# Kernel tuning notes

Measured on AMD Instinct MI355X. Metric: run time of the kernel, lower is better.

## Reference

```python
import jax, jax.numpy as jnp
import numpy as np

SEED_THRESHOLD = 0.5
DUPLICATE_THRESHOLD = 0.8


def setup_inputs() -> dict:
    key = jax.random.key(0)
    k1, k2 = jax.random.split(key)
    B, Q, C = 16, 1800, 256
    return {
        "query_signatures": jax.random.normal(k1, (B, Q, C), dtype=jnp.float32),
        "query_seed_logits": jax.random.normal(k2, (B, Q), dtype=jnp.float32),
    }


def _cc_labels(adj):
    """Connected-component labels via min-label propagation. adj: [Q,Q] bool (symmetric).
    Label of each node = smallest node index in its component. Unconnected nodes keep own index."""
    Q = adj.shape[0]
    labels0 = jnp.arange(Q, dtype=jnp.int32)

    def cond(state):
        return state[1]

    def body(state):
        labels, _ = state
        nbr_min = jnp.min(jnp.where(adj, labels[None, :], Q), axis=1)
        new = jnp.minimum(labels, nbr_min)
        return new, jnp.any(new != labels)

    labels, _ = jax.lax.while_loop(cond, body, (labels0, jnp.bool_(True)))
    return labels


def reference(query_signatures, query_seed_logits):
    sig = query_signatures                     # [B,Q,C]
    B, Q, C = sig.shape
    qidx = jnp.arange(Q)

    scores = jax.nn.sigmoid(query_seed_logits.astype(jnp.float32))   # [B,Q]
    selected = scores >= SEED_THRESHOLD                               # [B,Q]
    # fallback: if no query selected in an image, select the argmax-score query
    empty = ~jnp.any(selected, axis=1)                                # [B]
    fb = jnp.argmax(scores, axis=1)                                   # [B]
    selected = selected | (empty[:, None] & (qidx[None, :] == fb[:, None]))

    # cosine pairwise similarity
    nrm = jnp.linalg.norm(sig, axis=-1, keepdims=True)
    nsig = sig / jnp.maximum(nrm, 1e-12)
    sim = jnp.einsum("bqc,bkc->bqk", nsig, nsig)                      # [B,Q,Q]

    adj = (sim >= DUPLICATE_THRESHOLD) & selected[:, :, None] & selected[:, None, :]
    adj = adj.at[:, qidx, qidx].set(selected)                         # diag = selected

    labels = jax.vmap(_cc_labels)(adj)                                # [B,Q] int32

    # a label slot l hosts a component iff node l is selected and is its own component min
    active = selected & (labels == qidx[None, :].astype(labels.dtype))  # [B,Q]

    # per-component best-score member (components visited in ascending min-index order,
    # matching the torch BFS-from-ascending-node order)
    member = (labels[:, None, :] == qidx[None, :, None].astype(labels.dtype)) & selected[:, None, :]  # [B,Ql,Qn]
    masked_scores = jnp.where(member, scores[:, None, :], -jnp.inf)
    best = jnp.argmax(masked_scores, axis=2)                          # [B,Q] node index of best per label
    best_sig = jnp.take_along_axis(sig, best[..., None], axis=1)      # [B,Q,C]
    best_score = jnp.take_along_axis(scores, best, axis=1)            # [B,Q]

    # compact active components to the front (pad to Q, the static max)
    pos = jnp.cumsum(active, axis=1) - 1
    dest = jnp.where(active, pos, Q)                                  # inactive -> dropped

    seed_signatures = jax.vmap(
        lambda d, v: jnp.zeros((Q, C), sig.dtype).at[d].set(v, mode="drop")
    )(dest, best_sig)
    seed_scores = jax.vmap(
        lambda d, v: jnp.zeros((Q,), scores.dtype).at[d].set(v, mode="drop")
    )(dest, best_score)

    num_seeds = jnp.sum(active, axis=1)
    pad_mask = qidx[None, :] < num_seeds[:, None]
    return seed_signatures, pad_mask, seed_scores
```

## Files before the change

### kernel.cpp

```cpp
#include <hip/hip_runtime.h>
#include <hip/hip_bf16.h>
#include <stdint.h>

#define B_ 16
#define Q_ 1800
#define C_ 256
#define WPR 29
#define QPAD 1856
#define TBK 15
#define NTRI 120
#define OUT_SIG_ELEMS (B_*Q_*C_)

typedef unsigned long long u64;
typedef unsigned int u32;
typedef __attribute__((ext_vector_type(8))) short bf16x8;
typedef __attribute__((ext_vector_type(4))) float f32x4;

__global__ __launch_bounds__(256)
void k_compact(const float* __restrict__ logits,
               int* __restrict__ sel_idx, int* __restrict__ sel_cnt,
               int* __restrict__ dirty) {
  int b = blockIdx.x, t = threadIdx.x;
  int lane = t & 63, wid = t >> 6;
  __shared__ int wsum[4];
  __shared__ int s_tot;
  __shared__ u64 kw[4];
  const float* lgb = logits + b * Q_;
  if (t == 0) dirty[b] = 0;

  int f[8]; int cnt = 0;
  #pragma unroll
  for (int e = 0; e < 8; ++e) {
    int q = t * 8 + e; int fl = 0;
    if (q < Q_) fl = (lgb[q] >= 0.0f) ? 1 : 0;
    f[e] = fl; cnt += fl;
  }
  int incl = cnt;
  #pragma unroll
  for (int d = 1; d < 64; d <<= 1) {
    int v = __shfl_up(incl, d, 64);
    if (lane >= d) incl += v;
  }
  if (lane == 63) wsum[wid] = incl;
  __syncthreads();
  if (t == 0) {
    int acc = 0;
    #pragma unroll
    for (int i = 0; i < 4; ++i) { int v = wsum[i]; wsum[i] = acc; acc += v; }
    s_tot = acc;
  }
  __syncthreads();
  int excl = wsum[wid] + incl - cnt;
  int total = s_tot;

  if (total > 0) {
    #pragma unroll
    for (int e = 0; e < 8; ++e) {
      if (f[e]) { sel_idx[b * Q_ + excl] = t * 8 + e; excl++; }
    }
    if (t == 0) sel_cnt[b] = total;
  } else {
    u64 mk = 0;
    for (int q = t; q < Q_; q += 256) {
      float sc = 1.0f / (1.0f + expf(-lgb[q]));
      u64 key = ((u64)__float_as_uint(sc) << 32) | (u32)(~(u32)q);
      mk = (mk > key) ? mk : key;
    }
    #pragma unroll
    for (int d = 1; d < 64; d <<= 1) { u64 o = __shfl_xor(mk, d, 64); mk = (o > mk) ? o : mk; }
    if (lane == 0) kw[wid] = mk;
    __syncthreads();
    if (t == 0) {
      u64 m2 = kw[0];
      #pragma unroll
      for (int i = 1; i < 4; ++i) m2 = (kw[i] > m2) ? kw[i] : m2;
      sel_idx[b * Q_] = (int)(~(u32)m2);
      sel_cnt[b] = 1;
    }
  }
}

__global__ __launch_bounds__(256)
void k_prepg(const float* __restrict__ sig, const float* __restrict__ logits,
             const int* __restrict__ sel_idx, const int* __restrict__ sel_cnt,
             unsigned short* __restrict__ nsig, u32* __restrict__ rowmin,
             float* __restrict__ out_sig, float* __restrict__ out_mask,
             float* __restrict__ out_scores) {
  int b = blockIdx.y;
  int p = blockIdx.x * 4 + (threadIdx.x >> 6);
  int lane = threadIdx.x & 63;
  int S = sel_cnt[b];
  int Spad = (S + 63) & ~63;

  if (p < Spad && lane == 0) rowmin[b * QPAD + p] = 0xFFFFFFFFu;

  if (p < S) {
    int row = sel_idx[b * Q_ + p];
    const float* src = sig + ((size_t)b * Q_ + row) * C_;
    float4 v = *reinterpret_cast<const float4*>(src + lane * 4);

    float* orow = out_sig + ((size_t)b * Q_ + p) * C_;
    *reinterpret_cast<float4*>(orow + lane * 4) = v;
    if (lane == 0) {
      out_mask[b * Q_ + p] = 1.0f;
      out_scores[b * Q_ + p] = 1.0f / (1.0f + expf(-logits[b * Q_ + row]));
    }

    float ss = v.x * v.x + v.y * v.y + v.z * v.z + v.w * v.w;
    #pragma unroll
    for (int m = 32; m; m >>= 1) ss += __shfl_xor(ss, m, 64);
    float inv = 1.0f / fmaxf(sqrtf(ss), 1e-12f);
    __hip_bfloat16 h0 = __float2bfloat16(v.x * inv);
    __hip_bfloat16 h1 = __float2bfloat16(v.y * inv);
    __hip_bfloat16 h2 = __float2bfloat16(v.z * inv);
    __hip_bfloat16 h3 = __float2bfloat16(v.w * inv);
    unsigned short u0, u1, u2, u3;
    __builtin_memcpy(&u0, &h0, 2); __builtin_memcpy(&u1, &h1, 2);
    __builtin_memcpy(&u2, &h2, 2); __builtin_memcpy(&u3, &h3, 2);
    uint2 wv;
    wv.x = (u32)u0 | ((u32)u1 << 16);
    wv.y = (u32)u2 | ((u32)u3 << 16);
    *reinterpret_cast<uint2*>(nsig + ((size_t)b * QPAD + p) * C_ + lane * 4) = wv;
  } else {
    if (p < Spad)
      *reinterpret_cast<uint2*>(nsig + ((size_t)b * QPAD + p) * C_ + lane * 4) =
          make_uint2(0u, 0u);
    if (p < Q_) {
      float* orow = out_sig + ((size_t)b * Q_ + p) * C_;
      *reinterpret_cast<float4*>(orow + lane * 4) = make_float4(0.f, 0.f, 0.f, 0.f);
      if (lane == 0) {
        out_mask[b * Q_ + p] = 0.0f;
        out_scores[b * Q_ + p] = 0.0f;
      }
    }
  }
}

__global__ __launch_bounds__(256)
void k_prep(const float* __restrict__ sig, const int* __restrict__ sel_idx,
            const int* __restrict__ sel_cnt, unsigned short* __restrict__ nsig,
            u32* __restrict__ rowmin) {
  int b = blockIdx.y;
  int p = blockIdx.x * 4 + (threadIdx.x >> 6);
  int lane = threadIdx.x & 63;
  int S = sel_cnt[b];
  int Spad = (S + 63) & ~63;
  if (p >= Spad) return;
  if (lane == 0) rowmin[b * QPAD + p] = 0xFFFFFFFFu;
  unsigned short* dst = nsig + ((size_t)b * QPAD + p) * C_;
  if (p >= S) {
    *reinterpret_cast<uint2*>(dst + lane * 4) = make_uint2(0u, 0u);
    return;
  }
  int row = sel_idx[b * Q_ + p];
  const float* src = sig + ((size_t)b * Q_ + row) * C_;
  float4 v = *reinterpret_cast<const float4*>(src + lane * 4);
  float ss = v.x * v.x + v.y * v.y + v.z * v.z + v.w * v.w;
  #pragma unroll
  for (int m = 32; m; m >>= 1) ss += __shfl_xor(ss, m, 64);
  float inv = 1.0f / fmaxf(sqrtf(ss), 1e-12f);
  __hip_bfloat16 h0 = __float2bfloat16(v.x * inv);
  __hip_bfloat16 h1 = __float2bfloat16(v.y * inv);
  __hip_bfloat16 h2 = __float2bfloat16(v.z * inv);
  __hip_bfloat16 h3 = __float2bfloat16(v.w * inv);
  unsigned short u0, u1, u2, u3;
  __builtin_memcpy(&u0, &h0, 2); __builtin_memcpy(&u1, &h1, 2);
  __builtin_memcpy(&u2, &h2, 2); __builtin_memcpy(&u3, &h3, 2);
  uint2 wv;
  wv.x = (u32)u0 | ((u32)u1 << 16);
  wv.y = (u32)u2 | ((u32)u3 << 16);
  *reinterpret_cast<uint2*>(dst + lane * 4) = wv;
}

__global__ __launch_bounds__(256)
void k_sim(const unsigned short* __restrict__ nsig, const int* __restrict__ sel_cnt,
           u64* __restrict__ adj, u32* __restrict__ rowmin,
           int* __restrict__ dirty) {
  int lin = blockIdx.x;
  int b = lin & 15;
  int u = lin >> 4, tib = 0;
  while (u >= TBK - tib) { u -= TBK - tib; ++tib; }
  int tjb = tib + u;
  int S = sel_cnt[b];
  if (tjb * 128 >= S) return;
  const bool diag = (tib == tjb);

  __shared__ uint4 Alds[2048];
  __shared__ uint4 Blds[2048];
  __shared__ u64 adjtile[4][64];

  const int t = threadIdx.x;
  const int wv = t >> 6, lane = t & 63;
  const int lr = lane & 15, lg = lane >> 4;

  const int i1 = tib * 128 + (wv >> 1) * 64;
  const int j1 = tjb * 128 + (wv & 1) * 64;
  const bool live = (i1 < S) && (j1 < S);

  const char* gbase = (const char*)(nsig + (size_t)b * QPAD * C_);
  const char* arow = gbase + (size_t)tib * 128 * 512;
  const char* brow = gbase + (size_t)tjb * 128 * 512;

  f32x4 acc[4][4];
  #pragma unroll
  for (int rs = 0; rs < 4; ++rs)
    #pragma unroll
    for (int cg = 0; cg < 4; ++cg) acc[rs][cg] = (f32x4){0.f, 0.f, 0.f, 0.f};

  const int ra0 = (wv >> 1) * 64;
  const int rb0 = (wv & 1) * 64;
  const char* Bbase = reinterpret_cast<const char*>(diag ? Alds : Blds);

  for (int kh = 0; kh < 2; ++kh) {
    #pragma unroll
    for (int it = 0; it < 8; ++it) {
      int o = it * 4096 + t * 16;
      int r = o >> 8;
      int w = o & 255;
      int sw = o ^ ((r & 7) << 4);
      uint4 va = *reinterpret_cast<const uint4*>(arow + (size_t)r * 512 + kh * 256 + w);
      Alds[sw >> 4] = va;
      if (!diag) {
        uint4 vb = *reinterpret_cast<const uint4*>(brow + (size_t)r * 512 + kh * 256 + w);
        Blds[sw >> 4] = vb;
      }
    }
    __syncthreads();
    if (live) {
      #pragma unroll
      for (int ks = 0; ks < 4; ++ks) {
        bf16x8 af[4], bf[4];
        #pragma unroll
        for (int rs = 0; rs < 4; ++rs) {
          int r = ra0 + rs * 16 + lr;
          int byte = r * 256 + ((ks * 64 + lg * 16) ^ ((r & 7) << 4));
          af[rs] = *reinterpret_cast<const bf16x8*>(
              reinterpret_cast<const char*>(Alds) + byte);
        }
        #pragma unroll
        for (int cg = 0; cg < 4; ++cg) {
          int r = rb0 + cg * 16 + lr;
          int byte = r * 256 + ((ks * 64 + lg * 16) ^ ((r & 7) << 4));
          bf[cg] = *reinterpret_cast<const bf16x8*>(Bbase + byte);
        }
        #pragma unroll
        for (int rs = 0; rs < 4; ++rs)
          #pragma unroll
          for (int cg = 0; cg < 4; ++cg)
            acc[rs][cg] = __builtin_amdgcn_mfma_f32_16x16x32_bf16(
                af[rs], bf[cg], acc[rs][cg], 0, 0, 0);
      }
    }
    __syncthreads();
  }

  if (!live) return;
  adjtile[wv][lane] = 0ull;
  #pragma unroll
  for (int rs = 0; rs < 4; ++rs) {
    #pragma unroll
    for (int j = 0; j < 4; ++j) {
      u64 bits = 0ull;
      if (acc[rs][0][j] >= 0.8f) bits |= 1ull << (0  + lr);
      if (acc[rs][1][j] >= 0.8f) bits |= 1ull << (16 + lr);
      if (acc[rs][2][j] >= 0.8f) bits |= 1ull << (32 + lr);
      if (acc[rs][3][j] >= 0.8f) bits |= 1ull << (48 + lr);
      if (bits) atomicOr(&adjtile[wv][rs * 16 + lg * 4 + j], bits);
    }
  }
  int gi = i1 + lane;
  u64 word = adjtile[wv][lane];
  u64 selfbit = (i1 == j1) ? (1ull << lane) : 0ull;
  bool offd = (gi < S) && ((word & ~selfbit) != 0ull);
  if (__any(offd) && lane == 0) atomicOr(&dirty[b], 1);
  if (gi < S) {
    adj[((size_t)b * Q_ + gi) * WPR + (j1 >> 6)] = word;
    if (word) atomicMin(&rowmin[b * QPAD + gi], (u32)(j1 + __builtin_ctzll(word)));
  }
  if (!diag) {
    u64 tw = 0ull;
    for (int i = 0; i < 64; ++i)
      tw |= ((adjtile[wv][i] >> lane) & 1ull) << i;
    int gj = j1 + lane;
    if (gj < S) {
      adj[((size_t)b * Q_ + gj) * WPR + (i1 >> 6)] = tw;
      if (tw) atomicMin(&rowmin[b * QPAD + gj], (u32)(i1 + __builtin_ctzll(tw)));
    }
  }
}

__global__ __launch_bounds__(1024)
void k_fix(const float* __restrict__ sig, const float* __restrict__ logits,
           const int* __restrict__ sel_idx, const int* __restrict__ sel_cnt,
           const u64* __restrict__ adj, const u32* __restrict__ rowmin,
           const int* __restrict__ dirty,
           int* __restrict__ best_idx, float* __restrict__ best_sc,
           float* __restrict__ out_sig, float* __restrict__ out_mask,
           float* __restrict__ out_scores) {
  int b = blockIdx.x;
  if (!dirty[b]) return;
  int t = threadIdx.x;
  int lane = t & 63, wid = t >> 6;
  __shared__ int lab[Q_];
  __shared__ int lab2[Q_];
  __shared__ u64 best[Q_];
  __shared__ int wsum[16];
  __shared__ int s_tot;
  __shared__ int s_changed;

  int S = sel_cnt[b];
  int nw = (S + 63) >> 6;
  const u64* arow0 = adj + (size_t)b * Q_ * WPR;

  for (int s = t; s < S; s += 1024) {
    u32 m = rowmin[b * QPAD + s];
    lab[s] = (int)(((u32)s < m) ? (u32)s : m);
  }
  __syncthreads();
  for (int iter = 0; iter < Q_ + 2; ++iter) {
    if (t == 0) s_changed = 0;
    __syncthreads();
    for (int s = t; s < S; s += 1024) {
      int m = lab[s];
      const u64* row = arow0 + (size_t)s * WPR;
      for (int w = 0; w < nw; ++w) {
        u64 msk = row[w];
        while (msk) {
          int j = (w << 6) + __builtin_ctzll(msk);
          int lj = lab[j];
          m = (lj < m) ? lj : m;
          msk &= msk - 1;
        }
      }
      lab2[s] = m;
      if (m != lab[s]) s_changed = 1;
    }
    __syncthreads();
    int ch = s_changed;
    for (int s = t; s < S; s += 1024) lab[s] = lab2[s];
    __syncthreads();
    if (!ch) break;
  }

  for (int s = t; s < S; s += 1024) best[s] = 0ull;
  __syncthreads();
  const int* sidx = sel_idx + b * Q_;
  for (int s = t; s < S; s += 1024) {
    int orig = sidx[s];
    float sc = 1.0f / (1.0f + expf(-logits[b * Q_ + orig]));
    u64 key = ((u64)__float_as_uint(sc) << 32) | (u32)(~(u32)orig);
    atomicMax(&best[lab[s]], key);
  }
  __syncthreads();

  int f[2]; int cnt = 0;
  #pragma unroll
  for (int e = 0; e < 2; ++e) {
    int s = t * 2 + e;
    int fl = (s < S && lab[s] == s) ? 1 : 0;
    f[e] = fl; cnt += fl;
  }
  int incl = cnt;
  #pragma unroll
  for (int d = 1; d < 64; d <<= 1) {
    int v = __shfl_up(incl, d, 64);
    if (lane >= d) incl += v;
  }
  if (lane == 63) wsum[wid] = incl;
  __syncthreads();
  if (t == 0) {
    int acc = 0;
    #pragma unroll
    for (int i = 0; i < 16; ++i) { int v = wsum[i]; wsum[i] = acc; acc += v; }
    s_tot = acc;
  }
  __syncthreads();
  int excl = wsum[wid] + incl - cnt;
  #pragma unroll
  for (int e = 0; e < 2; ++e) {
    if (f[e]) {
      int s = t * 2 + e;
      u64 key = best[s];
      best_idx[b * Q_ + excl] = (int)(~(u32)key);
      best_sc[b * Q_ + excl] = __uint_as_float((u32)(key >> 32));
      excl++;
    }
  }
  __syncthreads();
  int n = s_tot;

  for (int p = wid; p < Q_; p += 16) {
    float* orow = out_sig + ((size_t)b * Q_ + p) * C_;
    if (p < n) {
      int row = best_idx[b * Q_ + p];
      float4 v = *reinterpret_cast<const float4*>(sig + ((size_t)b * Q_ + row) * C_ + lane * 4);
      *reinterpret_cast<float4*>(orow + lane * 4) = v;
      if (lane == 0) {
        out_mask[b * Q_ + p] = 1.0f;
        out_scores[b * Q_ + p] = best_sc[b * Q_ + p];
      }
    } else {
      *reinterpret_cast<float4*>(orow + lane * 4) = make_float4(0.f, 0.f, 0.f, 0.f);
      if (lane == 0) {
        out_mask[b * Q_ + p] = 0.0f;
        out_scores[b * Q_ + p] = 0.0f;
      }
    }
  }
}

__global__ __launch_bounds__(256)
void k_ccgather(const float* __restrict__ sig, const float* __restrict__ logits,
                const int* __restrict__ sel_idx, const int* __restrict__ sel_cnt,
                const u64* __restrict__ adj, const u32* __restrict__ rowmin,
                float* __restrict__ out_sig, float* __restrict__ out_mask,
                float* __restrict__ out_scores) {
  const int b = blockIdx.y, g = blockIdx.x;
  const int t = threadIdx.x, lane = t & 63, wid = t >> 6;
  __shared__ int lab[Q_];
  __shared__ int lab2[Q_];
  __shared__ u64 best[Q_];
  __shared__ int wsum[4];
  __shared__ int s_tot;
  __shared__ int s_dirty;

  const int S = sel_cnt[b];
  if (t == 0) s_dirty = 0;
  __syncthreads();
  for (int s = t; s < S; s += 256)
    if (rowmin[b * QPAD + s] != (u32)s) s_dirty = 1;
  __syncthreads();

  const int p = g * 4 + wid;
  float* orow = out_sig + ((size_t)b * Q_ + p) * C_;

  if (!s_dirty) {
    if (p < S) {
      int row = sel_idx[b * Q_ + p];
      float4 v = *reinterpret_cast<const float4*>(sig + ((size_t)b * Q_ + row) * C_ + lane * 4);
      *reinterpret_cast<float4*>(orow + lane * 4) = v;
      if (lane == 0) {
        out_mask[b * Q_ + p] = 1.0f;
        out_scores[b * Q_ + p] = 1.0f / (1.0f + expf(-logits[b * Q_ + row]));
      }
    } else {
      *reinterpret_cast<float4*>(orow + lane * 4) = make_float4(0.f, 0.f, 0.f, 0.f);
      if (lane == 0) {
        out_mask[b * Q_ + p] = 0.0f;
        out_scores[b * Q_ + p] = 0.0f;
      }
    }
    return;
  }

  const int nw = (S + 63) >> 6;
  const u64* arow0 = adj + (size_t)b * Q_ * WPR;
  __shared__ int s_chg;

  if (t == 0) s_chg = 1;
  for (int s = t; s < S; s += 256) {
    u32 m = rowmin[b * QPAD + s];
    lab[s] = (int)(((u32)s < m) ? (u32)s : m);
  }
  __syncthreads();
  for (int iter = 0; iter < Q_ + 2; ++iter) {
    if (t == 0) s_chg = 0;
    __syncthreads();
    for (int s = t; s < S; s += 256) {
      int m = lab[s];
      const u64* row = arow0 + (size_t)s * WPR;
      for (int w = 0; w < nw; ++w) {
        u64 msk = row[w];
        while (msk) {
          int j = (w << 6) + __builtin_ctzll(msk);
          int lj = lab[j];
          m = (lj < m) ? lj : m;
          msk &= msk - 1;
        }
      }
      lab2[s] = m;
      if (m != lab[s]) s_chg = 1;
    }
    __syncthreads();
    int ch = s_chg;
    for (int s = t; s < S; s += 256) lab[s] = lab2[s];
    __syncthreads();
    if (!ch) break;
  }

  for (int s = t; s < S; s += 256) best[s] = 0ull;
  __syncthreads();
  const int* sidx = sel_idx + b * Q_;
  for (int s = t; s < S; s += 256) {
    int orig = sidx[s];
    float sc = 1.0f / (1.0f + expf(-logits[b * Q_ + orig]));
    u64 key = ((u64)__float_as_uint(sc) << 32) | (u32)(~(u32)orig);
    atomicMax(&best[lab[s]], key);
  }
  __syncthreads();

  __shared__ int slot[4];
  int rf[8]; int rcnt = 0;
  #pragma unroll
  for (int e = 0; e < 8; ++e) {
    int s = t * 8 + e;
    int fl = (s < S && lab[s] == s) ? 1 : 0;
    rf[e] = fl; rcnt += fl;
  }
  int rincl = rcnt;
  #pragma unroll
  for (int d = 1; d < 64; d <<= 1) {
    int v = __shfl_up(rincl, d, 64);
    if (lane >= d) rincl += v;
  }
  if (t < 4) slot[t] = -1;
  if (lane == 63) wsum[wid] = rincl;
  __syncthreads();
  if (t == 0) {
    int acc = 0;
    #pragma unroll
    for (int i = 0; i < 4; ++i) { int v = wsum[i]; wsum[i] = acc; acc += v; }
    s_tot = acc;
  }
  __syncthreads();
  int rex = wsum[wid] + rincl - rcnt;
  #pragma unroll
  for (int e = 0; e < 8; ++e) {
    if (rf[e]) {
      if (rex >= g * 4 && rex < g * 4 + 4) slot[rex - g * 4] = t * 8 + e;
      rex++;
    }
  }
  __syncthreads();
  int n = s_tot;

  if (p < n) {
    u64 key = best[slot[wid]];
    int orig = (int)(~(u32)key);
    float4 v = *reinterpret_cast<const float4*>(sig + ((size_t)b * Q_ + orig) * C_ + lane * 4);
    *reinterpret_cast<float4*>(orow + lane * 4) = v;
    if (lane == 0) {
      out_mask[b * Q_ + p] = 1.0f;
      out_scores[b * Q_ + p] = __uint_as_float((u32)(key >> 32));
    }
  } else {
    *reinterpret_cast<float4*>(orow + lane * 4) = make_float4(0.f, 0.f, 0.f, 0.f);
    if (lane == 0) {
      out_mask[b * Q_ + p] = 0.0f;
      out_scores[b * Q_ + p] = 0.0f;
    }
  }
}

extern "C" void kernel_launch(void* const* d_in, const int* in_sizes, int n_in,
                              void* d_out, int out_size, void* d_ws, size_t ws_size,
                              hipStream_t stream) {
  const float* p0 = (const float*)d_in[0];
  const float* p1 = (const float*)d_in[1];
  const float* sig;  const float* logits;
  if (in_sizes[0] == B_ * Q_ * C_) { sig = p0; logits = p1; }
  else                             { sig = p1; logits = p0; }

  float* out = (float*)d_out;
  float* out_mask   = out + OUT_SIG_ELEMS;
  float* out_scores = out + OUT_SIG_ELEMS + B_ * Q_;

  char* w = (char*)d_ws;
  int* sel_cnt = (int*)w;  w += 256;
  int* dirty   = (int*)w;  w += 256;
  int* sel_idx = (int*)w;  w += B_ * Q_ * 4;

  dim3 gp(QPAD / 4, B_);
  dim3 gg(Q_ / 4, B_);

  const size_t need_A = 512 + 3 * (size_t)B_ * Q_ * 4 + (size_t)B_ * QPAD * 4 +
                        (size_t)B_ * Q_ * WPR * 8 + (size_t)B_ * QPAD * C_ * 2;
  const size_t need_B = 512 + (size_t)B_ * Q_ * 4 + (size_t)B_ * QPAD * 4 +
                        (size_t)B_ * Q_ * WPR * 8;

  if (ws_size >= need_A) {
    int* best_idx  = (int*)w;   w += B_ * Q_ * 4;
    float* best_sc = (float*)w; w += B_ * Q_ * 4;
    u32* rowmin = (u32*)w;      w += (size_t)B_ * QPAD * 4;
    u64* adj    = (u64*)w;      w += (size_t)B_ * Q_ * WPR * 8;
    unsigned short* nsig = (unsigned short*)w;

    k_compact<<<B_, 256, 0, stream>>>(logits, sel_idx, sel_cnt, dirty);
    k_prepg<<<gp, 256, 0, stream>>>(sig, logits, sel_idx, sel_cnt, nsig, rowmin,
                                    out, out_mask, out_scores);
    k_sim<<<B_ * NTRI, 256, 0, stream>>>(nsig, sel_cnt, adj, rowmin, dirty);
    k_fix<<<B_, 1024, 0, stream>>>(sig, logits, sel_idx, sel_cnt, adj, rowmin,
                                   dirty, best_idx, best_sc,
                                   out, out_mask, out_scores);
  } else if (ws_size >= need_B) {
    u32* rowmin = (u32*)w;  w += (size_t)B_ * QPAD * 4;
    u64* adj    = (u64*)w;
    unsigned short* nsig = (unsigned short*)((char*)d_out + (size_t)(8u << 20));

    k_compact<<<B_, 256, 0, stream>>>(logits, sel_idx, sel_cnt, dirty);
    k_prep<<<gp, 256, 0, stream>>>(sig, sel_idx, sel_cnt, nsig, rowmin);
    k_sim<<<B_ * NTRI, 256, 0, stream>>>(nsig, sel_cnt, adj, rowmin, dirty);
    k_ccgather<<<gg, 256, 0, stream>>>(sig, logits, sel_idx, sel_cnt, adj, rowmin,
                                       out, out_mask, out_scores);
  } else {
    u64* adj    = (u64*)d_out;
    u32* rowmin = (u32*)((char*)d_out + (size_t)(26u << 20));
    unsigned short* nsig = (unsigned short*)((char*)d_out + (size_t)(8u << 20));
    int* best_idx  = (int*)w;   w += B_ * Q_ * 4;
    float* best_sc = (float*)w;

    k_compact<<<B_, 256, 0, stream>>>(logits, sel_idx, sel_cnt, dirty);
    k_prep<<<gp, 256, 0, stream>>>(sig, sel_idx, sel_cnt, nsig, rowmin);
    k_sim<<<B_ * NTRI, 256, 0, stream>>>(nsig, sel_cnt, adj, rowmin, dirty);
    k_ccgather<<<gg, 256, 0, stream>>>(sig, logits, sel_idx, sel_cnt, adj, rowmin,
                                       out, out_mask, out_scores);
  }
}
```

Baseline: 39.54 us.

## Fuse selection compaction into the prep kernel, dropping one launch

Merges the per-image selection scan (k_compact) into the normalize/gather prep kernel. Each of 58 blocks per image redoes the 1800-element prefix scan and keeps only the 32 output slots it owns, so one kernel launch and the global sel_idx round-trip are gone. Prep now zero-pads nsig rows up to a multiple of 128 and k_sim guards loads past QPAD. The cost is redundant scan work in every block and fewer, larger blocks for the gather. The fallback paths for smaller workspaces are also adjusted.

```diff
diff --git a/kernel.cpp b/kernel.cpp
--- a/kernel.cpp
+++ b/kernel.cpp
@@ -10,6 +10,7 @@
 #define TBK 15
 #define NTRI 120
 #define OUT_SIG_ELEMS (B_*Q_*C_)
+#define NBPB 58
 
 typedef unsigned long long u64;
 typedef unsigned int u32;
@@ -17,17 +18,21 @@
 typedef __attribute__((ext_vector_type(4))) float f32x4;
 
 __global__ __launch_bounds__(256)
-void k_compact(const float* __restrict__ logits,
+void k_prepsel(const float* __restrict__ sig, const float* __restrict__ logits,
                int* __restrict__ sel_idx, int* __restrict__ sel_cnt,
-               int* __restrict__ dirty) {
-  int b = blockIdx.x, t = threadIdx.x;
-  int lane = t & 63, wid = t >> 6;
+               int* __restrict__ dirty,
+               unsigned short* __restrict__ nsig, u32* __restrict__ rowmin,
+               float* __restrict__ out_sig, float* __restrict__ out_mask,
+               float* __restrict__ out_scores) {
+  const int b = blockIdx.y, g = blockIdx.x;
+  const int t = threadIdx.x, lane = t & 63, wid = t >> 6;
+  const int p0 = g * 32;
   __shared__ int wsum[4];
+  __shared__ u64 kw[4];
   __shared__ int s_tot;
-  __shared__ u64 kw[4];
+  __shared__ int slot[32];
+
   const float* lgb = logits + b * Q_;
-  if (t == 0) dirty[b] = 0;
-
   int f[8]; int cnt = 0;
   #pragma unroll
   for (int e = 0; e < 8; ++e) {
@@ -50,16 +55,10 @@
     s_tot = acc;
   }
   __syncthreads();
-  int excl = wsum[wid] + incl - cnt;
-  int total = s_tot;
-
-  if (total > 0) {
-    #pragma unroll
-    for (int e = 0; e < 8; ++e) {
-      if (f[e]) { sel_idx[b * Q_ + excl] = t * 8 + e; excl++; }
-    }
-    if (t == 0) sel_cnt[b] = total;
-  } else {
+  int excl0 = wsum[wid] + incl - cnt;
+  int S = s_tot;
+  int fbq = -1;
+  if (S == 0) {
     u64 mk = 0;
     for (int q = t; q < Q_; q += 256) {
       float sc = 1.0f / (1.0f + expf(-lgb[q]));
@@ -70,106 +69,83 @@
     for (int d = 1; d < 64; d <<= 1) { u64 o = __shfl_xor(mk, d, 64); mk = (o > mk) ? o : mk; }
     if (lane == 0) kw[wid] = mk;
     __syncthreads();
-    if (t == 0) {
-      u64 m2 = kw[0];
+    u64 m2 = kw[0];
+    #pragma unroll
+    for (int i = 1; i < 4; ++i) m2 = (kw[i] > m2) ? kw[i] : m2;
+    fbq = (int)(~(u32)m2);
+    S = 1;
+  }
+  if (g == 0 && t == 0) { sel_cnt[b] = S; dirty[b] = 0; }
+
+  if (t < 32) slot[t] = -1;
+  __syncthreads();
+  if (fbq >= 0) {
+    if (g == 0 && t == 0) { slot[0] = fbq; sel_idx[b * Q_] = fbq; }
+  } else {
+    int ex = excl0;
+    #pragma unroll
+    for (int e = 0; e < 8; ++e) {
+      if (f[e]) {
+        int q = t * 8 + e;
+        if (ex >= p0 && ex < p0 + 32) {
+          slot[ex - p0] = q;
+          sel_idx[b * Q_ + ex] = q;
+        }
+        ex++;
+      }
+    }
+  }
+  __syncthreads();
+
+  const int Spad   = (S + 63) & ~63;
+  const int Spad128 = (S + 127) & ~127;
+
+  #pragma unroll
+  for (int r = 0; r < 8; ++r) {
+    int i = wid * 8 + r;
+    int p = p0 + i;
+    if (p < Spad && lane == 0) rowmin[b * QPAD + p] = 0xFFFFFFFFu;
+    if (p < S) {
+      int row = slot[i];
+      const float* src = sig + ((size_t)b * Q_ + row) * C_;
+      float4 v = *reinterpret_cast<const float4*>(src + lane * 4);
+
+      float* orow = out_sig + ((size_t)b * Q_ + p) * C_;
+      *reinterpret_cast<float4*>(orow + lane * 4) = v;
+      if (lane == 0) {
+        out_mask[b * Q_ + p] = 1.0f;
+        out_scores[b * Q_ + p] = 1.0f / (1.0f + expf(-lgb[row]));
+      }
+
+      float ss = v.x * v.x + v.y * v.y + v.z * v.z + v.w * v.w;
       #pragma unroll
-      for (int i = 1; i < 4; ++i) m2 = (kw[i] > m2) ? kw[i] : m2;
-      sel_idx[b * Q_] = (int)(~(u32)m2);
-      sel_cnt[b] = 1;
-    }
-  }
-}
-
-__global__ __launch_bounds__(256)
-void k_prepg(const float* __restrict__ sig, const float* __restrict__ logits,
-             const int* __restrict__ sel_idx, const int* __restrict__ sel_cnt,
-             unsigned short* __restrict__ nsig, u32* __restrict__ rowmin,
-             float* __restrict__ out_sig, float* __restrict__ out_mask,
-             float* __restrict__ out_scores) {
-  int b = blockIdx.y;
-  int p = blockIdx.x * 4 + (threadIdx.x >> 6);
-  int lane = threadIdx.x & 63;
-  int S = sel_cnt[b];
-  int Spad = (S + 63) & ~63;
-
-  if (p < Spad && lane == 0) rowmin[b * QPAD + p] = 0xFFFFFFFFu;
-
-  if (p < S) {
-    int row = sel_idx[b * Q_ + p];
-    const float* src = sig + ((size_t)b * Q_ + row) * C_;
-    float4 v = *reinterpret_cast<const float4*>(src + lane * 4);
-
-    float* orow = out_sig + ((size_t)b * Q_ + p) * C_;
-    *reinterpret_cast<float4*>(orow + lane * 4) = v;
-    if (lane == 0) {
-      out_mask[b * Q_ + p] = 1.0f;
-      out_scores[b * Q_ + p] = 1.0f / (1.0f + expf(-logits[b * Q_ + row]));
-    }
-
-    float ss = v.x * v.x + v.y * v.y + v.z * v.z + v.w * v.w;
-    #pragma unroll
-    for (int m = 32; m; m >>= 1) ss += __shfl_xor(ss, m, 64);
-    float inv = 1.0f / fmaxf(sqrtf(ss), 1e-12f);
-    __hip_bfloat16 h0 = __float2bfloat16(v.x * inv);
-    __hip_bfloat16 h1 = __float2bfloat16(v.y * inv);
-    __hip_bfloat16 h2 = __float2bfloat16(v.z * inv);
-    __hip_bfloat16 h3 = __float2bfloat16(v.w * inv);
-    unsigned short u0, u1, u2, u3;
-    __builtin_memcpy(&u0, &h0, 2); __builtin_memcpy(&u1, &h1, 2);
-    __builtin_memcpy(&u2, &h2, 2); __builtin_memcpy(&u3, &h3, 2);
-    uint2 wv;
-    wv.x = (u32)u0 | ((u32)u1 << 16);
-    wv.y = (u32)u2 | ((u32)u3 << 16);
-    *reinterpret_cast<uint2*>(nsig + ((size_t)b * QPAD + p) * C_ + lane * 4) = wv;
-  } else {
-    if (p < Spad)
-      *reinterpret_cast<uint2*>(nsig + ((size_t)b * QPAD + p) * C_ + lane * 4) =
-          make_uint2(0u, 0u);
-    if (p < Q_) {
-      float* orow = out_sig + ((size_t)b * Q_ + p) * C_;
-      *reinterpret_cast<float4*>(orow + lane * 4) = make_float4(0.f, 0.f, 0.f, 0.f);
-      if (lane == 0) {
-        out_mask[b * Q_ + p] = 0.0f;
-        out_scores[b * Q_ + p] = 0.0f;
-      }
-    }
-  }
-}
-
-__global__ __launch_bounds__(256)
-void k_prep(const float* __restrict__ sig, const int* __restrict__ sel_idx,
-            const int* __restrict__ sel_cnt, unsigned short* __restrict__ nsig,
-            u32* __restrict__ rowmin) {
-  int b = blockIdx.y;
-  int p = blockIdx.x * 4 + (threadIdx.x >> 6);
-  int lane = threadIdx.x & 63;
-  int S = sel_cnt[b];
-  int Spad = (S + 63) & ~63;
-  if (p >= Spad) return;
-  if (lane == 0) rowmin[b * QPAD + p] = 0xFFFFFFFFu;
-  unsigned short* dst = nsig + ((size_t)b * QPAD + p) * C_;
-  if (p >= S) {
-    *reinterpret_cast<uint2*>(dst + lane * 4) = make_uint2(0u, 0u);
-    return;
-  }
-  int row = sel_idx[b * Q_ + p];
-  const float* src = sig + ((size_t)b * Q_ + row) * C_;
-  float4 v = *reinterpret_cast<const float4*>(src + lane * 4);
-  float ss = v.x * v.x + v.y * v.y + v.z * v.z + v.w * v.w;
-  #pragma unroll
-  for (int m = 32; m; m >>= 1) ss += __shfl_xor(ss, m, 64);
-  float inv = 1.0f / fmaxf(sqrtf(ss), 1e-12f);
-  __hip_bfloat16 h0 = __float2bfloat16(v.x * inv);
-  __hip_bfloat16 h1 = __float2bfloat16(v.y * inv);
-  __hip_bfloat16 h2 = __float2bfloat16(v.z * inv);
-  __hip_bfloat16 h3 = __float2bfloat16(v.w * inv);
-  unsigned short u0, u1, u2, u3;
-  __builtin_memcpy(&u0, &h0, 2); __builtin_memcpy(&u1, &h1, 2);
-  __builtin_memcpy(&u2, &h2, 2); __builtin_memcpy(&u3, &h3, 2);
-  uint2 wv;
-  wv.x = (u32)u0 | ((u32)u1 << 16);
-  wv.y = (u32)u2 | ((u32)u3 << 16);
-  *reinterpret_cast<uint2*>(dst + lane * 4) = wv;
+      for (int m = 32; m; m >>= 1) ss += __shfl_xor(ss, m, 64);
+      float inv = 1.0f / fmaxf(sqrtf(ss), 1e-12f);
+      __hip_bfloat16 h0 = __float2bfloat16(v.x * inv);
+      __hip_bfloat16 h1 = __float2bfloat16(v.y * inv);
+      __hip_bfloat16 h2 = __float2bfloat16(v.z * inv);
+      __hip_bfloat16 h3 = __float2bfloat16(v.w * inv);
+      unsigned short u0, u1, u2, u3;
+      __builtin_memcpy(&u0, &h0, 2); __builtin_memcpy(&u1, &h1, 2);
+      __builtin_memcpy(&u2, &h2, 2); __builtin_memcpy(&u3, &h3, 2);
+      uint2 wv;
+      wv.x = (u32)u0 | ((u32)u1 << 16);
+      wv.y = (u32)u2 | ((u32)u3 << 16);
+      *reinterpret_cast<uint2*>(nsig + ((size_t)b * QPAD + p) * C_ + lane * 4) = wv;
+    } else {
+      if (p < Spad128)
+        *reinterpret_cast<uint2*>(nsig + ((size_t)b * QPAD + p) * C_ + lane * 4) =
+            make_uint2(0u, 0u);
+      if (p < Q_) {
+        float* orow = out_sig + ((size_t)b * Q_ + p) * C_;
+        *reinterpret_cast<float4*>(orow + lane * 4) = make_float4(0.f, 0.f, 0.f, 0.f);
+        if (lane == 0) {
+          out_mask[b * Q_ + p] = 0.0f;
+          out_scores[b * Q_ + p] = 0.0f;
+        }
+      }
+    }
+  }
 }
 
 __global__ __launch_bounds__(256)
@@ -218,10 +194,13 @@
       int r = o >> 8;
       int w = o & 255;
       int sw = o ^ ((r & 7) << 4);
-      uint4 va = *reinterpret_cast<const uint4*>(arow + (size_t)r * 512 + kh * 256 + w);
+      uint4 zz = make_uint4(0u, 0u, 0u, 0u);
+      uint4 va = (tib * 128 + r < QPAD)
+          ? *reinterpret_cast<const uint4*>(arow + (size_t)r * 512 + kh * 256 + w) : zz;
       Alds[sw >> 4] = va;
       if (!diag) {
-        uint4 vb = *reinterpret_cast<const uint4*>(brow + (size_t)r * 512 + kh * 256 + w);
+        uint4 vb = (tjb * 128 + r < QPAD)
+            ? *reinterpret_cast<const uint4*>(brow + (size_t)r * 512 + kh * 256 + w) : zz;
         Blds[sw >> 4] = vb;
       }
     }
@@ -410,6 +389,110 @@
 }
 
 __global__ __launch_bounds__(256)
+void k_compact(const float* __restrict__ logits,
+               int* __restrict__ sel_idx, int* __restrict__ sel_cnt,
+               int* __restrict__ dirty) {
+  int b = blockIdx.x, t = threadIdx.x;
+  int lane = t & 63, wid = t >> 6;
+  __shared__ int wsum[4];
+  __shared__ int s_tot;
+  __shared__ u64 kw[4];
+  const float* lgb = logits + b * Q_;
+  if (t == 0) dirty[b] = 0;
+
+  int f[8]; int cnt = 0;
+  #pragma unroll
+  for (int e = 0; e < 8; ++e) {
+    int q = t * 8 + e; int fl = 0;
+    if (q < Q_) fl = (lgb[q] >= 0.0f) ? 1 : 0;
+    f[e] = fl; cnt += fl;
+  }
+  int incl = cnt;
+  #pragma unroll
+  for (int d = 1; d < 64; d <<= 1) {
+    int v = __shfl_up(incl, d, 64);
+    if (lane >= d) incl += v;
+  }
+  if (lane == 63) wsum[wid] = incl;
+  __syncthreads();
+  if (t == 0) {
+    int acc = 0;
+    #pragma unroll
+    for (int i = 0; i < 4; ++i) { int v = wsum[i]; wsum[i] = acc; acc += v; }
+    s_tot = acc;
+  }
+  __syncthreads();
+  int excl = wsum[wid] + incl - cnt;
+  int total = s_tot;
+
+  if (total > 0) {
+    #pragma unroll
+    for (int e = 0; e < 8; ++e) {
+      if (f[e]) { sel_idx[b * Q_ + excl] = t * 8 + e; excl++; }
+    }
+    if (t == 0) sel_cnt[b] = total;
+  } else {
+    u64 mk = 0;
+    for (int q = t; q < Q_; q += 256) {
+      float sc = 1.0f / (1.0f + expf(-lgb[q]));
+      u64 key = ((u64)__float_as_uint(sc) << 32) | (u32)(~(u32)q);
+      mk = (mk > key) ? mk : key;
+    }
+    #pragma unroll
+    for (int d = 1; d < 64; d <<= 1) { u64 o = __shfl_xor(mk, d, 64); mk = (o > mk) ? o : mk; }
+    if (lane == 0) kw[wid] = mk;
+    __syncthreads();
+    if (t == 0) {
+      u64 m2 = kw[0];
+      #pragma unroll
+      for (int i = 1; i < 4; ++i) m2 = (kw[i] > m2) ? kw[i] : m2;
+      sel_idx[b * Q_] = (int)(~(u32)m2);
+      sel_cnt[b] = 1;
+    }
+  }
+}
+
+__global__ __launch_bounds__(256)
+void k_prep(const float* __restrict__ sig, const int* __restrict__ sel_idx,
+            const int* __restrict__ sel_cnt, unsigned short* __restrict__ nsig,
+            u32* __restrict__ rowmin) {
+  int b = blockIdx.y;
+  int p = blockIdx.x * 4 + (threadIdx.x >> 6);
+  int lane = threadIdx.x & 63;
+  int S = sel_cnt[b];
+  int Spad = (S + 63) & ~63;
+  int Spad128 = (S + 127) & ~127;
+  if (p >= Spad128 || p >= QPAD) {
+    if (p < Spad && lane == 0) rowmin[b * QPAD + p] = 0xFFFFFFFFu;
+    return;
+  }
+  if (p < Spad && lane == 0) rowmin[b * QPAD + p] = 0xFFFFFFFFu;
+  unsigned short* dst = nsig + ((size_t)b * QPAD + p) * C_;
+  if (p >= S) {
+    *reinterpret_cast<uint2*>(dst + lane * 4) = make_uint2(0u, 0u);
+    return;
+  }
+  int row = sel_idx[b * Q_ + p];
+  const float* src = sig + ((size_t)b * Q_ + row) * C_;
+  float4 v = *reinterpret_cast<const float4*>(src + lane * 4);
+  float ss = v.x * v.x + v.y * v.y + v.z * v.z + v.w * v.w;
+  #pragma unroll
+  for (int m = 32; m; m >>= 1) ss += __shfl_xor(ss, m, 64);
+  float inv = 1.0f / fmaxf(sqrtf(ss), 1e-12f);
+  __hip_bfloat16 h0 = __float2bfloat16(v.x * inv);
+  __hip_bfloat16 h1 = __float2bfloat16(v.y * inv);
+  __hip_bfloat16 h2 = __float2bfloat16(v.z * inv);
+  __hip_bfloat16 h3 = __float2bfloat16(v.w * inv);
+  unsigned short u0, u1, u2, u3;
+  __builtin_memcpy(&u0, &h0, 2); __builtin_memcpy(&u1, &h1, 2);
+  __builtin_memcpy(&u2, &h2, 2); __builtin_memcpy(&u3, &h3, 2);
+  uint2 wv;
+  wv.x = (u32)u0 | ((u32)u1 << 16);
+  wv.y = (u32)u2 | ((u32)u3 << 16);
+  *reinterpret_cast<uint2*>(dst + lane * 4) = wv;
+}
+
+__global__ __launch_bounds__(256)
 void k_ccgather(const float* __restrict__ sig, const float* __restrict__ logits,
                 const int* __restrict__ sel_idx, const int* __restrict__ sel_cnt,
                 const u64* __restrict__ adj, const u32* __restrict__ rowmin,
@@ -570,7 +653,6 @@
   int* dirty   = (int*)w;  w += 256;
   int* sel_idx = (int*)w;  w += B_ * Q_ * 4;
 
-  dim3 gp(QPAD / 4, B_);
   dim3 gg(Q_ / 4, B_);
 
   const size_t need_A = 512 + 3 * (size_t)B_ * Q_ * 4 + (size_t)B_ * QPAD * 4 +
@@ -585,9 +667,9 @@
     u64* adj    = (u64*)w;      w += (size_t)B_ * Q_ * WPR * 8;
     unsigned short* nsig = (unsigned short*)w;
 
-    k_compact<<<B_, 256, 0, stream>>>(logits, sel_idx, sel_cnt, dirty);
-    k_prepg<<<gp, 256, 0, stream>>>(sig, logits, sel_idx, sel_cnt, nsig, rowmin,
-                                    out, out_mask, out_scores);
+    dim3 gps(NBPB, B_);
+    k_prepsel<<<gps, 256, 0, stream>>>(sig, logits, sel_idx, sel_cnt, dirty,
+                                       nsig, rowmin, out, out_mask, out_scores);
     k_sim<<<B_ * NTRI, 256, 0, stream>>>(nsig, sel_cnt, adj, rowmin, dirty);
     k_fix<<<B_, 1024, 0, stream>>>(sig, logits, sel_idx, sel_cnt, adj, rowmin,
                                    dirty, best_idx, best_sc,
@@ -596,6 +678,7 @@
     u32* rowmin = (u32*)w;  w += (size_t)B_ * QPAD * 4;
     u64* adj    = (u64*)w;
     unsigned short* nsig = (unsigned short*)((char*)d_out + (size_t)(8u << 20));
+    dim3 gp(QPAD / 4, B_);
 
     k_compact<<<B_, 256, 0, stream>>>(logits, sel_idx, sel_cnt, dirty);
     k_prep<<<gp, 256, 0, stream>>>(sig, sel_idx, sel_cnt, nsig, rowmin);
@@ -604,10 +687,9 @@
                                        out, out_mask, out_scores);
   } else {
     u64* adj    = (u64*)d_out;
-    u32* rowmin = (u32*)((char*)d_out + (size_t)(26u << 20));
+    u32* rowmin = (u32*)w;
     unsigned short* nsig = (unsigned short*)((char*)d_out + (size_t)(8u << 20));
-    int* best_idx  = (int*)w;   w += B_ * Q_ * 4;
-    float* best_sc = (float*)w;
+    dim3 gp(QPAD / 4, B_);
 
     k_compact<<<B_, 256, 0, stream>>>(logits, sel_idx, sel_cnt, dirty);
     k_prep<<<gp, 256, 0, stream>>>(sig, sel_idx, sel_cnt, nsig, rowmin);
```

New measurement: 45.97 us. 16.3% more time.
